# Kernel optimization log

Hardware: AMD Instinct MI355X
Metric: run time of the kernel (lower is better)

The kernel has to match this reference:

```python
import jax, jax.numpy as jnp
import numpy as np

N = 8192
IN_C = 256
OUT_C = 64
ALPHA = 0.2  # LeakyReLU negative slope
NEG_INF = -9e15


def setup_inputs() -> dict:
    key = jax.random.key(0)
    k1, k2, k3, k4 = jax.random.split(key, 4)
    x = jax.random.normal(k1, (N, IN_C), dtype=jnp.float32)
    adjacent = jax.random.randint(k2, (N, N), 0, 2, dtype=jnp.int32)
    # xavier_uniform with gain=1.2: limit = gain * sqrt(6/(fan_in+fan_out))
    lim_w = 1.2 * np.sqrt(6.0 / (IN_C + OUT_C))
    w = jax.random.uniform(k3, (IN_C, OUT_C), dtype=jnp.float32, minval=-lim_w, maxval=lim_w)
    lim_a = 1.2 * np.sqrt(6.0 / (2 * OUT_C + 1))
    a = jax.random.uniform(k4, (2 * OUT_C, 1), dtype=jnp.float32, minval=-lim_a, maxval=lim_a)
    return {"x": x, "adjacent": adjacent, "w": w, "a": a}


def reference(x, adjacent, w, a):
    # h: [N, out]
    h = x @ w
    # e_ij = LeakyReLU(a^T [h_i || h_j]) computed without materializing [N,N,2*out]:
    # split a into source/target halves -> rank-1 broadcast sum.
    a_src = a[:OUT_C, 0]   # [out]
    a_dst = a[OUT_C:, 0]   # [out]
    f_src = h @ a_src      # [N]
    f_dst = h @ a_dst      # [N]
    e = f_src[:, None] + f_dst[None, :]            # [N, N]
    e = jnp.where(e > 0, e, ALPHA * e)             # LeakyReLU
    # mask by adjacency, softmax over neighbors (rows)
    e = jnp.where(adjacent > 0, e, NEG_INF)
    attention = jax.nn.softmax(e, axis=-1)         # [N, N]
    h_prime = attention @ h                        # [N, out]
    # concat=True -> ELU activation
    return jax.nn.elu(h_prime)
```

## Files before the change

### kernel.cpp

```cpp
#include <hip/hip_runtime.h>
#include <hip/hip_bf16.h>

#define N 8192
#define IN_C 256
#define OUT_C 64
#define ALPHA 0.2f
#define L2E 1.44269504f

typedef short bf16x8 __attribute__((ext_vector_type(8)));
typedef float f32x4 __attribute__((ext_vector_type(4)));
typedef unsigned long long u64;

#define OFF_H      0u
#define OFF_HT     2097152u
#define OFF_FS     3145728u
#define OFF_FD     3178496u
#define OFF_FDMAX  3211264u
#define OFF_BITS   3211520u
#define OFF_NUM    11600128u

__global__ __launch_bounds__(256) void k_linear(const float* __restrict__ x,
                                                const float* __restrict__ w,
                                                const float* __restrict__ a,
                                                float* __restrict__ h,
                                                float* __restrict__ fs,
                                                float* __restrict__ fd) {
    __shared__ float wl[IN_C * OUT_C];
    int t = threadIdx.x;
    for (int idx = t; idx < IN_C * OUT_C; idx += 256) wl[idx] = w[idx];
    __syncthreads();
    int i = blockIdx.x * 4 + (t >> 6);
    int c = t & 63;
    const float* xr = x + (size_t)i * IN_C;
    float acc = 0.f;
#pragma unroll 8
    for (int k = 0; k < IN_C; ++k) acc = fmaf(xr[k], wl[k * 64 + c], acc);
    h[(size_t)i * 64 + c] = acc;
    float s = acc * a[c];
    float d = acc * a[64 + c];
#pragma unroll
    for (int off = 32; off > 0; off >>= 1) {
        s += __shfl_xor(s, off, 64);
        d += __shfl_xor(d, off, 64);
    }
    if (c == 0) { fs[i] = s; fd[i] = d; }
}

__global__ __launch_bounds__(256) void k_frag(const float* __restrict__ h,
                                              unsigned short* __restrict__ htf) {
    __shared__ float lds[64 * 65];
    int t = threadIdx.x;
    int i0 = blockIdx.x * 64;
#pragma unroll
    for (int k = 0; k < 16; ++k) {
        int idx = k * 256 + t;
        int il = idx >> 6, c = idx & 63;
        lds[c * 65 + il] = h[(size_t)(i0 + il) * 64 + c];
    }
    __syncthreads();
    int l = t & 63;
    int ct = t >> 6;
    int r = l & 15, kg = l >> 4;
    int ch = ct * 16 + r;
#pragma unroll
    for (int ksl = 0; ksl < 2; ++ksl) {
        int ks = blockIdx.x * 2 + ksl;
        int n0 = ksl * 32 + kg * 8;
        bf16x8 v;
#pragma unroll
        for (int e = 0; e < 8; ++e) {
            __hip_bfloat16 hb = __float2bfloat16(lds[ch * 65 + n0 + e]);
            union { __hip_bfloat16 b; short s16; } u; u.b = hb;
            v[e] = u.s16;
        }
        *(bf16x8*)(htf + ((size_t)(ks * 4 + ct) * 64 + l) * 8) = v;
    }
}

__global__ __launch_bounds__(256) void k_fdmax(const float* __restrict__ fd,
                                               float* __restrict__ out) {
    __shared__ float red[256];
    int t = threadIdx.x;
    float m = -3.4e38f;
    for (int j = t; j < N; j += 256) m = fmaxf(m, fd[j]);
    red[t] = m;
    __syncthreads();
    for (int s = 128; s > 0; s >>= 1) {
        if (t < s) red[t] = fmaxf(red[t], red[t + s]);
        __syncthreads();
    }
    if (t == 0) out[0] = red[0];
}

__global__ __launch_bounds__(256) void k_pack(const int* __restrict__ adj,
                                              u64* __restrict__ bits) {
    int t = threadIdx.x, l = t & 63;
    int wv = (blockIdx.x * 256 + t) >> 6;
    const int NWV = 2048 * 4;
#pragma unroll 1
    for (int base = wv * 4; base < 262144; base += NWV * 4) {
        int4 v0 = *(const int4*)(adj + (size_t)(base + 0) * 256 + l * 4);
        int4 v1 = *(const int4*)(adj + (size_t)(base + 1) * 256 + l * 4);
        int4 v2 = *(const int4*)(adj + (size_t)(base + 2) * 256 + l * 4);
        int4 v3 = *(const int4*)(adj + (size_t)(base + 3) * 256 + l * 4);
        u64 b00 = __ballot(v0.x > 0), b01 = __ballot(v0.y > 0);
        u64 b02 = __ballot(v0.z > 0), b03 = __ballot(v0.w > 0);
        u64 b10 = __ballot(v1.x > 0), b11 = __ballot(v1.y > 0);
        u64 b12 = __ballot(v1.z > 0), b13 = __ballot(v1.w > 0);
        u64 b20 = __ballot(v2.x > 0), b21 = __ballot(v2.y > 0);
        u64 b22 = __ballot(v2.z > 0), b23 = __ballot(v2.w > 0);
        u64 b30 = __ballot(v3.x > 0), b31 = __ballot(v3.y > 0);
        u64 b32 = __ballot(v3.z > 0), b33 = __ballot(v3.w > 0);
        if (l == 0) {
            u64* q = bits + (size_t)base * 4;
            q[0] = b00; q[1] = b01; q[2]  = b02; q[3]  = b03;
            q[4] = b10; q[5] = b11; q[6]  = b12; q[7]  = b13;
            q[8] = b20; q[9] = b21; q[10] = b22; q[11] = b23;
            q[12] = b30; q[13] = b31; q[14] = b32; q[15] = b33;
        }
    }
}

__device__ __forceinline__ void stage16(const unsigned short* g, unsigned short* lds) {
    __builtin_amdgcn_global_load_lds(
        (const __attribute__((address_space(1))) unsigned int*)g,
        (__attribute__((address_space(3))) unsigned int*)lds, 16, 0, 0);
}

__global__ __launch_bounds__(256, 4) void k_mfma(
    const u64* __restrict__ bitsg,
    const float* __restrict__ fsrc,
    const float* __restrict__ fdst,
    const float* __restrict__ fdmax_p,
    const unsigned short* __restrict__ htf,
    float* __restrict__ nump,
    float* __restrict__ denp_out,
    int jch, int ns, int groups) {
    __shared__ u64 bits[64 * 34];
    __shared__ float fd_lds[1024];
    __shared__ alignas(16) unsigned short bufs[4][2048];
    int bid = blockIdx.x;
    int rb = bid & 127, kq = bid >> 7;
    int t = threadIdx.x, w = t >> 6, l = t & 63;
    int r = l & 15, kg = l >> 4, kg2 = kg * 2;
    int ib0 = rb * 64;
    int i = ib0 + w * 16 + r;
    int j0 = kq * jch;
    int strideU = groups * 4 + 2;
    int gw = groups * 4;
    int gbase4 = (j0 >> 8) * 4;
    bool fdl = (jch <= 1024);

    for (int u = t; u < 64 * gw; u += 256) {
        int rowL = u / gw, rem = u - rowL * gw;
        bits[rowL * strideU + rem] = bitsg[(size_t)(ib0 + rowL) * 128 + gbase4 + rem];
    }
    if (fdl) for (int u = t; u < jch; u += 256) fd_lds[u] = fdst[j0 + u];
    __syncthreads();

    float fs  = fsrc[i];
    float fdm = *fdmax_p;
    float e0  = fs + fdm;
    float m   = fmaxf(e0, ALPHA * e0);
    float mL  = m * L2E;

    int ks0 = j0 >> 5;
    stage16(htf + ((size_t)(ks0 + 0) * 2048 + t * 8), &bufs[0][w * 512]);
    stage16(htf + ((size_t)(ks0 + 1) * 2048 + t * 8), &bufs[1][w * 512]);
    stage16(htf + ((size_t)(ks0 + 2) * 2048 + t * 8), &bufs[2][w * 512]);

    bf16x8 bones;
#pragma unroll
    for (int e = 0; e < 8; ++e) bones[e] = (short)0x3F80;

    f32x4 acc0 = {0.f,0.f,0.f,0.f}, acc1 = {0.f,0.f,0.f,0.f};
    f32x4 acc2 = {0.f,0.f,0.f,0.f}, acc3 = {0.f,0.f,0.f,0.f};
    f32x4 acc4 = {0.f,0.f,0.f,0.f};

    int rowL = w * 16 + r;
#pragma unroll 1
    for (int g = 0; g < groups; ++g) {
        const u64* mp = &bits[rowL * strideU + g * 4];
        u64 m0 = mp[0], m1 = mp[1], m2 = mp[2], m3 = mp[3];
        u64 msel[4] = {m0, m1, m2, m3};
#pragma unroll
        for (int k8 = 0; k8 < 8; ++k8) {
            int ks = g * 8 + k8;
            if (ks < ns - 2)       asm volatile("s_waitcnt vmcnt(2)" ::: "memory");
            else if (ks == ns - 2) asm volatile("s_waitcnt vmcnt(1)" ::: "memory");
            else                   asm volatile("s_waitcnt vmcnt(0)" ::: "memory");
            asm volatile("s_barrier" ::: "memory");
            if (ks + 3 < ns)
                stage16(htf + ((size_t)(ks0 + ks + 3) * 2048 + t * 8),
                        &bufs[(ks + 3) & 3][w * 512]);

            const unsigned short* bp = &bufs[ks & 3][0];
            bf16x8 b0 = *(const bf16x8*)(bp + (0 * 64 + l) * 8);
            bf16x8 b1 = *(const bf16x8*)(bp + (1 * 64 + l) * 8);
            bf16x8 b2 = *(const bf16x8*)(bp + (2 * 64 + l) * 8);
            bf16x8 b3 = *(const bf16x8*)(bp + (3 * 64 + l) * 8);
            float4 fd0, fd1;
            if (fdl) {
                fd0 = *(const float4*)(fd_lds + ks * 32 + kg * 8);
                fd1 = *(const float4*)(fd_lds + ks * 32 + kg * 8 + 4);
            } else {
                fd0 = *(const float4*)(fdst + j0 + ks * 32 + kg * 8);
                fd1 = *(const float4*)(fdst + j0 + ks * 32 + kg * 8 + 4);
            }
            float fdv[8] = {fd0.x, fd0.y, fd0.z, fd0.w, fd1.x, fd1.y, fd1.z, fd1.w};
            bf16x8 af;
#pragma unroll
            for (int e = 0; e < 8; ++e) {
                int sh = k8 * 8 + kg2 + (e >> 2);
                unsigned bit = (unsigned)(msel[e & 3] >> sh) & 1u;
                float ee = fs + fdv[e];
                float lv = fmaxf(ee, ALPHA * ee);
                float a2 = __builtin_fmaf(lv, L2E, -mL);
                float wt = __builtin_amdgcn_exp2f(a2);
                wt = bit ? wt : 0.f;
                __hip_bfloat16 hb = __float2bfloat16(wt);
                union { __hip_bfloat16 b; short s16; } u; u.b = hb;
                af[e] = u.s16;
            }
            acc0 = __builtin_amdgcn_mfma_f32_16x16x32_bf16(af, b0, acc0, 0, 0, 0);
            acc1 = __builtin_amdgcn_mfma_f32_16x16x32_bf16(af, b1, acc1, 0, 0, 0);
            acc2 = __builtin_amdgcn_mfma_f32_16x16x32_bf16(af, b2, acc2, 0, 0, 0);
            acc3 = __builtin_amdgcn_mfma_f32_16x16x32_bf16(af, b3, acc3, 0, 0, 0);
            acc4 = __builtin_amdgcn_mfma_f32_16x16x32_bf16(af, bones, acc4, 0, 0, 0);
        }
    }

    int orow = ib0 + w * 16 + kg * 4;
    float* np = nump + (size_t)kq * N * 64;
#pragma unroll
    for (int rr = 0; rr < 4; ++rr) {
        np[(size_t)(orow + rr) * 64 + 0 * 16 + r] = acc0[rr];
        np[(size_t)(orow + rr) * 64 + 1 * 16 + r] = acc1[rr];
        np[(size_t)(orow + rr) * 64 + 2 * 16 + r] = acc2[rr];
        np[(size_t)(orow + rr) * 64 + 3 * 16 + r] = acc3[rr];
    }
    if (r == 0) {
#pragma unroll
        for (int rr = 0; rr < 4; ++rr) denp_out[kq * N + orow + rr] = acc4[rr];
    }
}

__global__ __launch_bounds__(256) void k_final(const float* __restrict__ nump,
                                               const float* __restrict__ denp,
                                               float* __restrict__ out,
                                               int kqn) {
    int gid = blockIdx.x * 256 + threadIdx.x;
    int base = gid * 4;
    int i = base >> 6;
    float4 num = {0.f, 0.f, 0.f, 0.f};
    float den = 0.f;
    for (int q = 0; q < kqn; ++q) {
        float4 v = *(const float4*)(nump + (size_t)q * (N * 64) + base);
        num.x += v.x; num.y += v.y; num.z += v.z; num.w += v.w;
        den += denp[q * N + i];
    }
    float rd = 1.f / den;
    float4 o;
    o.x = num.x * rd; o.y = num.y * rd; o.z = num.z * rd; o.w = num.w * rd;
    o.x = o.x > 0.f ? o.x : __expf(o.x) - 1.f;
    o.y = o.y > 0.f ? o.y : __expf(o.y) - 1.f;
    o.z = o.z > 0.f ? o.z : __expf(o.z) - 1.f;
    o.w = o.w > 0.f ? o.w : __expf(o.w) - 1.f;
    *(float4*)(out + base) = o;
}

extern "C" void kernel_launch(void* const* d_in, const int* in_sizes, int n_in,
                              void* d_out, int out_size, void* d_ws, size_t ws_size,
                              hipStream_t stream) {
    const float* x   = (const float*)d_in[0];
    const int*   adj = (const int*)d_in[1];
    const float* w   = (const float*)d_in[2];
    const float* a   = (const float*)d_in[3];
    float* out = (float*)d_out;
    char*  ws  = (char*)d_ws;

    float*          h    = (float*)(ws + OFF_H);
    unsigned short* htf  = (unsigned short*)(ws + OFF_HT);
    float*          fs   = (float*)(ws + OFF_FS);
    float*          fd   = (float*)(ws + OFF_FD);
    float*          fdm  = (float*)(ws + OFF_FDMAX);
    u64*            bits = (u64*)(ws + OFF_BITS);
    float*          nump = (float*)(ws + OFF_NUM);

    size_t need8 = (size_t)OFF_NUM + 8ull * N * 64 * 4 + 8ull * N * 4;
    int KQ = (ws_size >= need8) ? 8 : 4;
    float* denp = nump + (size_t)KQ * N * 64;
    int jch = N / KQ;
    int ns  = jch / 32;
    int groups = jch / 256;

    k_linear<<<2048, 256, 0, stream>>>(x, w, a, h, fs, fd);
    k_frag<<<128, 256, 0, stream>>>(h, htf);
    k_fdmax<<<1, 256, 0, stream>>>(fd, fdm);
    k_pack<<<2048, 256, 0, stream>>>(adj, bits);
    k_mfma<<<KQ * 128, 256, 0, stream>>>(bits, fs, fd, fdm, htf, nump, denp,
                                         jch, ns, groups);
    k_final<<<512, 256, 0, stream>>>(nump, denp, out, KQ);
}
```

Baseline: 500.4 us.

## Fuse adjacency bit-packing into the attention MFMA kernel

Removes the separate k_pack kernel and its global bitmask buffer. Each k_gat block now reads its own 64x1024 slice of the int adjacency matrix, ballots it into bitmasks directly in LDS, and then runs the MFMA attention loop. The chunk count is also hard-coded to 8 with compile-time constants, which drops the runtime workspace-size check and the global-memory fd fallback. This saves one launch and the bitmask write and readback, but the large adjacency read now sits in the kernel prologue, before the pipelined loop starts.

New measurement: 461.2 us. 7.8% less time.

```diff
diff --git a/kernel.cpp b/kernel.cpp
--- a/kernel.cpp
+++ b/kernel.cpp
@@ -6,6 +6,11 @@
 #define OUT_C 64
 #define ALPHA 0.2f
 #define L2E 1.44269504f
+#define KQ 8
+#define JCH 1024
+#define NS 32
+#define GROUPS 4
+#define STRIDEU 19
 
 typedef short bf16x8 __attribute__((ext_vector_type(8)));
 typedef float f32x4 __attribute__((ext_vector_type(4)));
@@ -16,8 +21,7 @@
 #define OFF_FS     3145728u
 #define OFF_FD     3178496u
 #define OFF_FDMAX  3211264u
-#define OFF_BITS   3211520u
-#define OFF_NUM    11600128u
+#define OFF_NUM    3211520u
 
 __global__ __launch_bounds__(256) void k_linear(const float* __restrict__ x,
                                                 const float* __restrict__ w,
@@ -92,52 +96,22 @@
     if (t == 0) out[0] = red[0];
 }
 
-__global__ __launch_bounds__(256) void k_pack(const int* __restrict__ adj,
-                                              u64* __restrict__ bits) {
-    int t = threadIdx.x, l = t & 63;
-    int wv = (blockIdx.x * 256 + t) >> 6;
-    const int NWV = 2048 * 4;
-#pragma unroll 1
-    for (int base = wv * 4; base < 262144; base += NWV * 4) {
-        int4 v0 = *(const int4*)(adj + (size_t)(base + 0) * 256 + l * 4);
-        int4 v1 = *(const int4*)(adj + (size_t)(base + 1) * 256 + l * 4);
-        int4 v2 = *(const int4*)(adj + (size_t)(base + 2) * 256 + l * 4);
-        int4 v3 = *(const int4*)(adj + (size_t)(base + 3) * 256 + l * 4);
-        u64 b00 = __ballot(v0.x > 0), b01 = __ballot(v0.y > 0);
-        u64 b02 = __ballot(v0.z > 0), b03 = __ballot(v0.w > 0);
-        u64 b10 = __ballot(v1.x > 0), b11 = __ballot(v1.y > 0);
-        u64 b12 = __ballot(v1.z > 0), b13 = __ballot(v1.w > 0);
-        u64 b20 = __ballot(v2.x > 0), b21 = __ballot(v2.y > 0);
-        u64 b22 = __ballot(v2.z > 0), b23 = __ballot(v2.w > 0);
-        u64 b30 = __ballot(v3.x > 0), b31 = __ballot(v3.y > 0);
-        u64 b32 = __ballot(v3.z > 0), b33 = __ballot(v3.w > 0);
-        if (l == 0) {
-            u64* q = bits + (size_t)base * 4;
-            q[0] = b00; q[1] = b01; q[2]  = b02; q[3]  = b03;
-            q[4] = b10; q[5] = b11; q[6]  = b12; q[7]  = b13;
-            q[8] = b20; q[9] = b21; q[10] = b22; q[11] = b23;
-            q[12] = b30; q[13] = b31; q[14] = b32; q[15] = b33;
-        }
-    }
-}
-
 __device__ __forceinline__ void stage16(const unsigned short* g, unsigned short* lds) {
     __builtin_amdgcn_global_load_lds(
         (const __attribute__((address_space(1))) unsigned int*)g,
         (__attribute__((address_space(3))) unsigned int*)lds, 16, 0, 0);
 }
 
-__global__ __launch_bounds__(256, 4) void k_mfma(
-    const u64* __restrict__ bitsg,
+__global__ __launch_bounds__(256, 4) void k_gat(
+    const int* __restrict__ adj,
     const float* __restrict__ fsrc,
     const float* __restrict__ fdst,
     const float* __restrict__ fdmax_p,
     const unsigned short* __restrict__ htf,
     float* __restrict__ nump,
-    float* __restrict__ denp_out,
-    int jch, int ns, int groups) {
-    __shared__ u64 bits[64 * 34];
-    __shared__ float fd_lds[1024];
+    float* __restrict__ denp_out) {
+    __shared__ u64 bits[64 * STRIDEU];
+    __shared__ float fd_lds[JCH];
     __shared__ alignas(16) unsigned short bufs[4][2048];
     int bid = blockIdx.x;
     int rb = bid & 127, kq = bid >> 7;
@@ -145,17 +119,47 @@
     int r = l & 15, kg = l >> 4, kg2 = kg * 2;
     int ib0 = rb * 64;
     int i = ib0 + w * 16 + r;
-    int j0 = kq * jch;
-    int strideU = groups * 4 + 2;
-    int gw = groups * 4;
-    int gbase4 = (j0 >> 8) * 4;
-    bool fdl = (jch <= 1024);
-
-    for (int u = t; u < 64 * gw; u += 256) {
-        int rowL = u / gw, rem = u - rowL * gw;
-        bits[rowL * strideU + rem] = bitsg[(size_t)(ib0 + rowL) * 128 + gbase4 + rem];
-    }
-    if (fdl) for (int u = t; u < jch; u += 256) fd_lds[u] = fdst[j0 + u];
+    int j0 = kq * JCH;
+
+    for (int u = t; u < JCH; u += 256) fd_lds[u] = fdst[j0 + u];
+
+#pragma unroll 1
+    for (int rr = 0; rr < 16; rr += 2) {
+        int rA = w * 16 + rr, rB = rA + 1;
+        const int* sA = adj + (size_t)(ib0 + rA) * N + j0;
+        const int* sB = adj + (size_t)(ib0 + rB) * N + j0;
+        int4 va[GROUPS], vb[GROUPS];
+#pragma unroll
+        for (int g = 0; g < GROUPS; ++g) va[g] = *(const int4*)(sA + g * 256 + l * 4);
+#pragma unroll
+        for (int g = 0; g < GROUPS; ++g) vb[g] = *(const int4*)(sB + g * 256 + l * 4);
+        u64 mA[16];
+#pragma unroll
+        for (int g = 0; g < GROUPS; ++g) {
+            mA[g * 4 + 0] = __ballot(va[g].x > 0);
+            mA[g * 4 + 1] = __ballot(va[g].y > 0);
+            mA[g * 4 + 2] = __ballot(va[g].z > 0);
+            mA[g * 4 + 3] = __ballot(va[g].w > 0);
+        }
+        if (l == 0) {
+            u64* p = &bits[rA * STRIDEU];
+#pragma unroll
+            for (int q = 0; q < 16; ++q) p[q] = mA[q];
+        }
+        u64 mB[16];
+#pragma unroll
+        for (int g = 0; g < GROUPS; ++g) {
+            mB[g * 4 + 0] = __ballot(vb[g].x > 0);
+            mB[g * 4 + 1] = __ballot(vb[g].y > 0);
+            mB[g * 4 + 2] = __ballot(vb[g].z > 0);
+            mB[g * 4 + 3] = __ballot(vb[g].w > 0);
+        }
+        if (l == 0) {
+            u64* p = &bits[rB * STRIDEU];
+#pragma unroll
+            for (int q = 0; q < 16; ++q) p[q] = mB[q];
+        }
+    }
     __syncthreads();
 
     float fs  = fsrc[i];
@@ -179,18 +183,18 @@
 
     int rowL = w * 16 + r;
 #pragma unroll 1
-    for (int g = 0; g < groups; ++g) {
-        const u64* mp = &bits[rowL * strideU + g * 4];
+    for (int g = 0; g < GROUPS; ++g) {
+        const u64* mp = &bits[rowL * STRIDEU + g * 4];
         u64 m0 = mp[0], m1 = mp[1], m2 = mp[2], m3 = mp[3];
         u64 msel[4] = {m0, m1, m2, m3};
 #pragma unroll
         for (int k8 = 0; k8 < 8; ++k8) {
             int ks = g * 8 + k8;
-            if (ks < ns - 2)       asm volatile("s_waitcnt vmcnt(2)" ::: "memory");
-            else if (ks == ns - 2) asm volatile("s_waitcnt vmcnt(1)" ::: "memory");
+            if (ks < NS - 2)       asm volatile("s_waitcnt vmcnt(2)" ::: "memory");
+            else if (ks == NS - 2) asm volatile("s_waitcnt vmcnt(1)" ::: "memory");
             else                   asm volatile("s_waitcnt vmcnt(0)" ::: "memory");
             asm volatile("s_barrier" ::: "memory");
-            if (ks + 3 < ns)
+            if (ks + 3 < NS)
                 stage16(htf + ((size_t)(ks0 + ks + 3) * 2048 + t * 8),
                         &bufs[(ks + 3) & 3][w * 512]);
 
@@ -199,14 +203,8 @@
             bf16x8 b1 = *(const bf16x8*)(bp + (1 * 64 + l) * 8);
             bf16x8 b2 = *(const bf16x8*)(bp + (2 * 64 + l) * 8);
             bf16x8 b3 = *(const bf16x8*)(bp + (3 * 64 + l) * 8);
-            float4 fd0, fd1;
-            if (fdl) {
-                fd0 = *(const float4*)(fd_lds + ks * 32 + kg * 8);
-                fd1 = *(const float4*)(fd_lds + ks * 32 + kg * 8 + 4);
-            } else {
-                fd0 = *(const float4*)(fdst + j0 + ks * 32 + kg * 8);
-                fd1 = *(const float4*)(fdst + j0 + ks * 32 + kg * 8 + 4);
-            }
+            float4 fd0 = *(const float4*)(fd_lds + ks * 32 + kg * 8);
+            float4 fd1 = *(const float4*)(fd_lds + ks * 32 + kg * 8 + 4);
             float fdv[8] = {fd0.x, fd0.y, fd0.z, fd0.w, fd1.x, fd1.y, fd1.z, fd1.w};
             bf16x8 af;
 #pragma unroll
@@ -247,14 +245,14 @@
 
 __global__ __launch_bounds__(256) void k_final(const float* __restrict__ nump,
                                                const float* __restrict__ denp,
-                                               float* __restrict__ out,
-                                               int kqn) {
+                                               float* __restrict__ out) {
     int gid = blockIdx.x * 256 + threadIdx.x;
     int base = gid * 4;
     int i = base >> 6;
     float4 num = {0.f, 0.f, 0.f, 0.f};
     float den = 0.f;
-    for (int q = 0; q < kqn; ++q) {
+#pragma unroll
+    for (int q = 0; q < KQ; ++q) {
         float4 v = *(const float4*)(nump + (size_t)q * (N * 64) + base);
         num.x += v.x; num.y += v.y; num.z += v.z; num.w += v.w;
         den += denp[q * N + i];
@@ -284,21 +282,12 @@
     float*          fs   = (float*)(ws + OFF_FS);
     float*          fd   = (float*)(ws + OFF_FD);
     float*          fdm  = (float*)(ws + OFF_FDMAX);
-    u64*            bits = (u64*)(ws + OFF_BITS);
     float*          nump = (float*)(ws + OFF_NUM);
-
-    size_t need8 = (size_t)OFF_NUM + 8ull * N * 64 * 4 + 8ull * N * 4;
-    int KQ = (ws_size >= need8) ? 8 : 4;
-    float* denp = nump + (size_t)KQ * N * 64;
-    int jch = N / KQ;
-    int ns  = jch / 32;
-    int groups = jch / 256;
+    float*          denp = nump + (size_t)KQ * N * 64;
 
     k_linear<<<2048, 256, 0, stream>>>(x, w, a, h, fs, fd);
     k_frag<<<128, 256, 0, stream>>>(h, htf);
     k_fdmax<<<1, 256, 0, stream>>>(fd, fdm);
-    k_pack<<<2048, 256, 0, stream>>>(adj, bits);
-    k_mfma<<<KQ * 128, 256, 0, stream>>>(bits, fs, fd, fdm, htf, nump, denp,
-                                         jch, ns, groups);
-    k_final<<<512, 256, 0, stream>>>(nump, denp, out, KQ);
-}
+    k_gat<<<KQ * 128, 256, 0, stream>>>(adj, fs, fd, fdm, htf, nump, denp);
+    k_final<<<512, 256, 0, stream>>>(nump, denp, out);
+}
```
